# Kernel tuning notes

Hardware: AMD Instinct MI355X
Metric: run time of the kernel (lower is better)

## Reference

```python
import jax, jax.numpy as jnp
import numpy as np

N_SRC0, N_DST0 = 200000, 50000
N_DST1 = 10000
D_IN, D_HID = 128, 128


def _sage_mean(h, src, dst, n_dst, W_self, b_self, W_neigh, b_neigh, act):
    # gather messages from src nodes, mean-aggregate per dst node
    msg = h[src]                                             # [E, D]
    agg = jax.ops.segment_sum(msg, dst, num_segments=n_dst)  # [n_dst, D]
    deg = jax.ops.segment_sum(jnp.ones(dst.shape, h.dtype), dst, num_segments=n_dst)
    h_neigh = agg / jnp.maximum(deg, 1.0)[:, None]
    # DGL block convention: dst nodes are the first n_dst src nodes
    rst = h[:n_dst] @ W_self + b_self + h_neigh @ W_neigh + b_neigh
    return jax.nn.relu(rst) if act else rst


def setup_inputs() -> dict:
    key = jax.random.key(0)
    ks = jax.random.split(key, 12)
    s = 1.0 / np.sqrt(D_HID)
    return {
        "features": jax.random.normal(ks[0], (N_SRC0, D_IN), jnp.float32),
        "src0": jax.random.randint(ks[1], (800000,), 0, N_SRC0),
        "dst0": jax.random.randint(ks[2], (800000,), 0, N_DST0),
        "src1": jax.random.randint(ks[3], (160000,), 0, N_DST0),
        "dst1": jax.random.randint(ks[4], (160000,), 0, N_DST1),
        "W_init": jax.random.uniform(ks[5], (D_IN, D_HID), jnp.float32, -s, s),
        "b_init": jax.random.uniform(ks[6], (D_HID,), jnp.float32, -s, s),
        "W_self": jax.random.uniform(ks[7], (D_HID, D_HID), jnp.float32, -s, s),
        "b_self": jax.random.uniform(ks[8], (D_HID,), jnp.float32, -s, s),
        "W_neigh": jax.random.uniform(ks[9], (D_HID, D_HID), jnp.float32, -s, s),
        "b_neigh": jax.random.uniform(ks[10], (D_HID,), jnp.float32, -s, s),
    }


def reference(features, src0, dst0, src1, dst1, W_init, b_init, W_self, b_self, W_neigh, b_neigh):
    # fc_init + activation
    h = jax.nn.relu(features @ W_init + b_init)              # [N_SRC0, D_HID]
    # block 0 (act_flag True), dropout p=0.0 is identity
    h = _sage_mean(h, src0, dst0, N_DST0, W_self, b_self, W_neigh, b_neigh, act=True)
    # block 1 (last block: act_flag False)
    h = _sage_mean(h, src1, dst1, N_DST1, W_self, b_self, W_neigh, b_neigh, act=False)
    return jnp.squeeze(h, axis=1) if h.shape[1] == 1 else h  # h.squeeze(1) no-op for D_HID>1
```

## Files before the change

kernel.cpp:

```cpp
#include <hip/hip_runtime.h>
#include <stdint.h>
#include <stddef.h>


#define DIM 128
constexpr int N_SRC0 = 200000;
constexpr int N_DST0 = 50000;
constexpr int N_DST1 = 10000;
constexpr int E0 = 800000;
constexpr int E1 = 160000;
constexpr int MAXDEG = 64;

constexpr int FC_BLOCKS = 1024;
constexpr int PLACE_BLOCKS = 1024;

typedef __attribute__((ext_vector_type(8))) short bf16x8;
typedef __attribute__((ext_vector_type(4))) float f32x4;

__device__ __forceinline__ uint16_t f2bf(float f) {
  union { float f; uint32_t u; } v; v.f = f;
  return (uint16_t)((v.u + 0x7FFFu + ((v.u >> 16) & 1u)) >> 16);
}
__device__ __forceinline__ float bf2f(uint16_t h) {
  union { uint32_t u; float f; } v; v.u = ((uint32_t)h) << 16;
  return v.f;
}

__global__ __launch_bounds__(256, 4) void place_fc_kernel(
    const int* __restrict__ src0, const int* __restrict__ dst0,
    const int* __restrict__ src1, const int* __restrict__ dst1,
    int* __restrict__ cnt0, int* __restrict__ cnt1,
    int* __restrict__ eslot0, int* __restrict__ eslot1,
    const float* __restrict__ feat, const float* __restrict__ W_init,
    const float* __restrict__ bias, uint16_t* __restrict__ hout) {
  __shared__ __align__(16) float tile[2][4096];

  if ((blockIdx.x & 1) == 0) {
    int pb = blockIdx.x >> 1;
    int part = pb & 7;
    int bpp  = PLACE_BLOCKS >> 3;
    int bidx = pb >> 3;
    const int4* s04 = (const int4*)src0;
    const int4* d04 = (const int4*)dst0;
    const int4* s14 = (const int4*)src1;
    const int4* d14 = (const int4*)dst1;

    int lo = part * (N_DST0 / 8), hi = lo + (N_DST0 / 8);
    for (int i = bidx * 256 + threadIdx.x; i < E0 / 4; i += bpp * 256) {
      int4 d = d04[i]; int4 s = s04[i];
      if (d.x >= lo && d.x < hi) { int p = atomicAdd(&cnt0[d.x], 1); if (p < MAXDEG) eslot0[(size_t)d.x * MAXDEG + p] = s.x; }
      if (d.y >= lo && d.y < hi) { int p = atomicAdd(&cnt0[d.y], 1); if (p < MAXDEG) eslot0[(size_t)d.y * MAXDEG + p] = s.y; }
      if (d.z >= lo && d.z < hi) { int p = atomicAdd(&cnt0[d.z], 1); if (p < MAXDEG) eslot0[(size_t)d.z * MAXDEG + p] = s.z; }
      if (d.w >= lo && d.w < hi) { int p = atomicAdd(&cnt0[d.w], 1); if (p < MAXDEG) eslot0[(size_t)d.w * MAXDEG + p] = s.w; }
    }
    int lo1 = part * (N_DST1 / 8), hi1 = lo1 + (N_DST1 / 8);
    for (int i = bidx * 256 + threadIdx.x; i < E1 / 4; i += bpp * 256) {
      int4 d = d14[i]; int4 s = s14[i];
      if (d.x >= lo1 && d.x < hi1) { int p = atomicAdd(&cnt1[d.x], 1); if (p < MAXDEG) eslot1[(size_t)d.x * MAXDEG + p] = s.x; }
      if (d.y >= lo1 && d.y < hi1) { int p = atomicAdd(&cnt1[d.y], 1); if (p < MAXDEG) eslot1[(size_t)d.y * MAXDEG + p] = s.y; }
      if (d.z >= lo1 && d.z < hi1) { int p = atomicAdd(&cnt1[d.z], 1); if (p < MAXDEG) eslot1[(size_t)d.z * MAXDEG + p] = s.z; }
      if (d.w >= lo1 && d.w < hi1) { int p = atomicAdd(&cnt1[d.w], 1); if (p < MAXDEG) eslot1[(size_t)d.w * MAXDEG + p] = s.w; }
    }
    return;
  }

  const int tid = threadIdx.x;
  const int w = tid >> 6, lane = tid & 63;
  const int q = lane >> 4, m16 = lane & 15;
  const int sl = w >> 1, nh = w & 1;

  {
    uint16_t* wtmp = (uint16_t*)tile;
    for (int u = 0; u < 8; u++) {
      int c = u * 256 + tid;
      int lane_c = c & 63;
      int nt = (c >> 6) & 7;
      int kc = c >> 9;
      int k0 = kc * 32 + (lane_c >> 4) * 8;
      int n  = nt * 16 + (lane_c & 15);
      bf16x8 frag;
#pragma unroll
      for (int j = 0; j < 8; j++)
        frag[j] = (short)f2bf(W_init[(size_t)(k0 + j) * DIM + n]);
      *(bf16x8*)&wtmp[(size_t)c * 8] = frag;
    }
  }
  __syncthreads();

  bf16x8 wv[4][4];
  {
    const uint16_t* wtmp = (const uint16_t*)tile;
#pragma unroll
    for (int kc = 0; kc < 4; kc++)
#pragma unroll
      for (int jj = 0; jj < 4; jj++)
        wv[kc][jj] = *(const bf16x8*)&wtmp[((kc * 8 + nh * 4 + jj) * 64 + lane) * 8];
  }
  __syncthreads();

  float bv[4];
#pragma unroll
  for (int j = 0; j < 4; j++) bv[j] = bias[(nh * 4 + j) * 16 + m16];

  const int ntiles = N_SRC0 / 32;

  const int lrow0 = w * 8 + (lane >> 5);
  auto stage = [&](int t, int buf) {
#pragma unroll
    for (int i = 0; i < 4; i++) {
      int row = lrow0 + i * 2;
      int g = (lane & 31) ^ (row & 7);
      const float* gs = feat + (size_t)t * 4096 + row * 128 + g * 4;
      float* ld = &tile[buf][w * 1024 + i * 256];
      __builtin_amdgcn_global_load_lds(
          (const __attribute__((address_space(1))) uint32_t*)gs,
          (__attribute__((address_space(3))) uint32_t*)ld,
          16, 0, 0);
    }
  };

  int t = blockIdx.x >> 1;
  int cur = 0;
  if (t < ntiles) stage(t, 0);
  __syncthreads();

  const int trow = sl * 16 + m16;
  const int sw = trow & 7;

  while (t < ntiles) {
    int tn = t + FC_BLOCKS;
    if (tn < ntiles) stage(tn, cur ^ 1);

    f32x4 acc[4];
#pragma unroll
    for (int j = 0; j < 4; j++) acc[j] = (f32x4){0.f, 0.f, 0.f, 0.f};

    const char* rb = (const char*)&tile[cur][0] + trow * 512;
#pragma unroll
    for (int kc = 0; kc < 4; kc++) {
      int g0 = kc * 8 + q * 2;
      float4 x0 = *(const float4*)(rb + ((g0    ) ^ sw) * 16);
      float4 x1 = *(const float4*)(rb + ((g0 + 1) ^ sw) * 16);
      bf16x8 a;
      a[0] = (short)f2bf(x0.x); a[1] = (short)f2bf(x0.y);
      a[2] = (short)f2bf(x0.z); a[3] = (short)f2bf(x0.w);
      a[4] = (short)f2bf(x1.x); a[5] = (short)f2bf(x1.y);
      a[6] = (short)f2bf(x1.z); a[7] = (short)f2bf(x1.w);
#pragma unroll
      for (int j = 0; j < 4; j++)
        acc[j] = __builtin_amdgcn_mfma_f32_16x16x32_bf16(a, wv[kc][j], acc[j], 0, 0, 0);
    }

    int rowb = t * 32 + sl * 16 + q * 4;
#pragma unroll
    for (int j = 0; j < 4; j++)
#pragma unroll
      for (int r = 0; r < 4; r++) {
        float v = fmaxf(acc[j][r] + bv[j], 0.f);
        hout[(size_t)(rowb + r) * DIM + (nh * 4 + j) * 16 + m16] = f2bf(v);
      }

    __syncthreads();
    cur ^= 1;
    t = tn;
  }
}

__global__ __launch_bounds__(256) void agg_kernel(
    const int* __restrict__ eslot, const int* __restrict__ deg,
    const uint16_t* __restrict__ hsrc, uint16_t* __restrict__ hout, int n_dst,
    const float* __restrict__ WS_src, const float* __restrict__ WN_src,
    uint16_t* __restrict__ Wf_out) {
  int nagg = n_dst >> 2;
  if (blockIdx.x >= nagg) {
    int pid = (blockIdx.x - nagg) * 256 + threadIdx.x;
#pragma unroll
    for (int u = 0; u < 4; u++) {
      int gid = pid * 4 + u;
      int m = gid >> 14, idx = gid & 16383;
      const float* W = m ? WN_src : WS_src;
      int j = idx & 7, lane = (idx >> 3) & 63, nt = (idx >> 9) & 7, kc = idx >> 12;
      int k = kc * 32 + (lane >> 4) * 8 + j;
      int n = nt * 16 + (lane & 15);
      Wf_out[gid] = f2bf(W[k * DIM + n]);
    }
    return;
  }

  int d = (blockIdx.x * 256 + threadIdx.x) >> 6;
  int lane = threadIdx.x & 63;
  if (d >= n_dst) return;
  const int* sl = eslot + (size_t)d * MAXDEG;
  int dg = deg[d];
  int dgc = dg < MAXDEG ? dg : MAXDEG;
  int qr = lane >> 4;
  int c  = lane & 15;

  float a0 = 0.f, a1 = 0.f, a2 = 0.f, a3 = 0.f;
  float a4 = 0.f, a5 = 0.f, a6 = 0.f, a7 = 0.f;

#define ACC4(P)                                                          \
  a0 += bf2f((uint16_t)(P).x); a1 += bf2f((uint16_t)((P).x >> 16));      \
  a2 += bf2f((uint16_t)(P).y); a3 += bf2f((uint16_t)((P).y >> 16));      \
  a4 += bf2f((uint16_t)(P).z); a5 += bf2f((uint16_t)((P).z >> 16));      \
  a6 += bf2f((uint16_t)(P).w); a7 += bf2f((uint16_t)((P).w >> 16));

  int e = 0;
  for (; e + 16 <= dgc; e += 16) {
    int s0 = sl[e + qr];
    int s1 = sl[e + 4 + qr];
    int s2 = sl[e + 8 + qr];
    int s3 = sl[e + 12 + qr];
    uint4 p0 = *(const uint4*)(hsrc + (size_t)s0 * DIM + c * 8);
    uint4 p1 = *(const uint4*)(hsrc + (size_t)s1 * DIM + c * 8);
    uint4 p2 = *(const uint4*)(hsrc + (size_t)s2 * DIM + c * 8);
    uint4 p3 = *(const uint4*)(hsrc + (size_t)s3 * DIM + c * 8);
    ACC4(p0); ACC4(p1); ACC4(p2); ACC4(p3);
  }
  for (; e + 8 <= dgc; e += 8) {
    int s0 = sl[e + qr];
    int s1 = sl[e + 4 + qr];
    uint4 p0 = *(const uint4*)(hsrc + (size_t)s0 * DIM + c * 8);
    uint4 p1 = *(const uint4*)(hsrc + (size_t)s1 * DIM + c * 8);
    ACC4(p0); ACC4(p1);
  }
  for (; e + 4 <= dgc; e += 4) {
    int s0 = sl[e + qr];
    uint4 p0 = *(const uint4*)(hsrc + (size_t)s0 * DIM + c * 8);
    ACC4(p0);
  }
  int rem = dgc - e;
  if (qr < rem) {
    int s0 = sl[e + qr];
    uint4 p0 = *(const uint4*)(hsrc + (size_t)s0 * DIM + c * 8);
    ACC4(p0);
  }
#undef ACC4

  a0 += __shfl_xor(a0, 16); a0 += __shfl_xor(a0, 32);
  a1 += __shfl_xor(a1, 16); a1 += __shfl_xor(a1, 32);
  a2 += __shfl_xor(a2, 16); a2 += __shfl_xor(a2, 32);
  a3 += __shfl_xor(a3, 16); a3 += __shfl_xor(a3, 32);
  a4 += __shfl_xor(a4, 16); a4 += __shfl_xor(a4, 32);
  a5 += __shfl_xor(a5, 16); a5 += __shfl_xor(a5, 32);
  a6 += __shfl_xor(a6, 16); a6 += __shfl_xor(a6, 32);
  a7 += __shfl_xor(a7, 16); a7 += __shfl_xor(a7, 32);

  if (qr == 0) {
    float inv = 1.f / fmaxf((float)dg, 1.f);
    uint4 o;
    o.x = (uint32_t)f2bf(a0 * inv) | ((uint32_t)f2bf(a1 * inv) << 16);
    o.y = (uint32_t)f2bf(a2 * inv) | ((uint32_t)f2bf(a3 * inv) << 16);
    o.z = (uint32_t)f2bf(a4 * inv) | ((uint32_t)f2bf(a5 * inv) << 16);
    o.w = (uint32_t)f2bf(a6 * inv) | ((uint32_t)f2bf(a7 * inv) << 16);
    *(uint4*)(hout + (size_t)d * DIM + c * 8) = o;
  }
}

template <bool ACT, bool OUT_BF16>
__global__ __launch_bounds__(256) void sage_kernel(
    const uint16_t* __restrict__ hself, const uint16_t* __restrict__ hneigh,
    const uint16_t* __restrict__ WfS, const uint16_t* __restrict__ WfN,
    const float* __restrict__ bS, const float* __restrict__ bN,
    void* __restrict__ outp, int n_dst) {
  __shared__ uint16_t wS[16384];
  __shared__ uint16_t wN[16384];
  {
    const uint4* gS = (const uint4*)WfS;
    const uint4* gN = (const uint4*)WfN;
    uint4* sS = (uint4*)wS;
    uint4* sN = (uint4*)wN;
    for (int i = threadIdx.x; i < 2048; i += 256) { sS[i] = gS[i]; sN[i] = gN[i]; }
  }
  __syncthreads();

  int wave = (blockIdx.x * 256 + threadIdx.x) >> 6;
  int nwaves = (gridDim.x * 256) >> 6;
  int lane = threadIdx.x & 63;
  int q = lane >> 4, m16 = lane & 15;

  float bv[8];
#pragma unroll
  for (int nt = 0; nt < 8; nt++)
    bv[nt] = bS[nt * 16 + m16] + bN[nt * 16 + m16];

  const int nstrips = n_dst / 16;
  int s = wave;
  bf16x8 XS[4], XN[4];
  if (s < nstrips) {
    size_t ro = (size_t)(s * 16 + m16) * DIM + q * 8;
#pragma unroll
    for (int kc = 0; kc < 4; kc++) {
      XS[kc] = *(const bf16x8*)(hself + ro + kc * 32);
      XN[kc] = *(const bf16x8*)(hneigh + ro + kc * 32);
    }
  }

  while (s < nstrips) {
    int sn = s + nwaves;
    bf16x8 YS[4], YN[4];
    if (sn < nstrips) {
      size_t ro = (size_t)(sn * 16 + m16) * DIM + q * 8;
#pragma unroll
      for (int kc = 0; kc < 4; kc++) {
        YS[kc] = *(const bf16x8*)(hself + ro + kc * 32);
        YN[kc] = *(const bf16x8*)(hneigh + ro + kc * 32);
      }
    }

    f32x4 acc[8];
#pragma unroll
    for (int nt = 0; nt < 8; nt++) acc[nt] = (f32x4){0.f, 0.f, 0.f, 0.f};

#pragma unroll
    for (int kc = 0; kc < 4; kc++) {
#pragma unroll
      for (int nt = 0; nt < 8; nt++) {
        size_t fo = (size_t)((kc * 8 + nt) * 64 + lane) * 8;
        bf16x8 ws = *(const bf16x8*)&wS[fo];
        bf16x8 wn = *(const bf16x8*)&wN[fo];
        acc[nt] = __builtin_amdgcn_mfma_f32_16x16x32_bf16(XS[kc], ws, acc[nt], 0, 0, 0);
        acc[nt] = __builtin_amdgcn_mfma_f32_16x16x32_bf16(XN[kc], wn, acc[nt], 0, 0, 0);
      }
    }

    int m0 = s * 16;
#pragma unroll
    for (int nt = 0; nt < 8; nt++)
#pragma unroll
      for (int r = 0; r < 4; r++) {
        float v = acc[nt][r] + bv[nt];
        if (ACT) v = fmaxf(v, 0.f);
        size_t o = (size_t)(m0 + q * 4 + r) * DIM + nt * 16 + m16;
        if (OUT_BF16) ((uint16_t*)outp)[o] = f2bf(v);
        else          ((float*)outp)[o] = v;
      }

#pragma unroll
    for (int i = 0; i < 4; i++) { XS[i] = YS[i]; XN[i] = YN[i]; }
    s = sn;
  }
}

extern "C" void kernel_launch(void* const* d_in, const int* in_sizes, int n_in,
                              void* d_out, int out_size, void* d_ws, size_t ws_size,
                              hipStream_t stream) {
  const float* feat   = (const float*)d_in[0];
  const int* src0     = (const int*)d_in[1];
  const int* dst0     = (const int*)d_in[2];
  const int* src1     = (const int*)d_in[3];
  const int* dst1     = (const int*)d_in[4];
  const float* W_init = (const float*)d_in[5];
  const float* b_init = (const float*)d_in[6];
  const float* W_self = (const float*)d_in[7];
  const float* b_self = (const float*)d_in[8];
  const float* W_neigh= (const float*)d_in[9];
  const float* b_neigh= (const float*)d_in[10];

  char* ws = (char*)d_ws;
  uint16_t* h     = (uint16_t*)(ws + 0);
  uint16_t* h1    = (uint16_t*)(ws + 51200000);
  uint16_t* hn    = (uint16_t*)(ws + 64000000);
  int*      cnt0  = (int*)(ws + 76800000);
  int*      cnt1  = (int*)(ws + 77000000);
  int*      eslot0= (int*)(ws + 77040000);
  int*      eslot1= (int*)(ws + 89840000);
  uint16_t* WfI   = (uint16_t*)(ws + 92400000);
  uint16_t* WfS   = WfI + 16384;
  uint16_t* WfN   = WfS + 16384;

  hipMemsetAsync(ws + 76800000, 0, 240000, stream);

  place_fc_kernel<<<PLACE_BLOCKS + FC_BLOCKS, 256, 0, stream>>>(
      src0, dst0, src1, dst1, cnt0, cnt1, eslot0, eslot1,
      feat, W_init, b_init, h);

  agg_kernel<<<N_DST0 / 4 + 32, 256, 0, stream>>>(eslot0, cnt0, h, hn, N_DST0,
                                                  W_self, W_neigh, WfS);
  sage_kernel<true, true><<<782, 256, 0, stream>>>(h, hn, WfS, WfN, b_self, b_neigh,
                                                   h1, N_DST0);

  agg_kernel<<<N_DST1 / 4, 256, 0, stream>>>(eslot1, cnt1, h1, hn, N_DST1,
                                             nullptr, nullptr, nullptr);
  sage_kernel<false, false><<<157, 256, 0, stream>>>(h1, hn, WfS, WfN, b_self, b_neigh,
                                                     d_out, N_DST1);
}
```

Measured before the change: 273.2 us.

## Fuse neighbor aggregation with SAGE matmul and move weight prep into FC kernel

Merges the separate aggregation and SAGE linear kernels into one kernel per layer. Each block aggregates 16 destination rows into a swizzled LDS tile and immediately runs the MFMA projection against global pre-swizzled weights, so the intermediate neighbor-mean buffer never makes a round trip through HBM. Weight conversion to bf16 fragment layout moves into extra blocks of the first place/FC kernel. The FC loop also replaces __syncthreads with explicit vmcnt waits plus raw barriers so the prefetch of the next tile can stay in flight. The trade-offs are that weights are now read from global memory per block rather than staged in LDS, and each wave computes only two output column tiles.

```diff
diff --git a/kernel.cpp b/kernel.cpp
--- a/kernel.cpp
+++ b/kernel.cpp
@@ -13,6 +13,7 @@
 
 constexpr int FC_BLOCKS = 1024;
 constexpr int PLACE_BLOCKS = 1024;
+constexpr int PREP_BLOCKS = 16;
 
 typedef __attribute__((ext_vector_type(8))) short bf16x8;
 typedef __attribute__((ext_vector_type(4))) float f32x4;
@@ -32,8 +33,25 @@
     int* __restrict__ cnt0, int* __restrict__ cnt1,
     int* __restrict__ eslot0, int* __restrict__ eslot1,
     const float* __restrict__ feat, const float* __restrict__ W_init,
-    const float* __restrict__ bias, uint16_t* __restrict__ hout) {
+    const float* __restrict__ bias, uint16_t* __restrict__ hout,
+    const float* __restrict__ WS_src, const float* __restrict__ WN_src,
+    uint16_t* __restrict__ Wf_out) {
   __shared__ __align__(16) float tile[2][4096];
+
+  if (blockIdx.x >= PLACE_BLOCKS + FC_BLOCKS) {
+    int pid = (blockIdx.x - (PLACE_BLOCKS + FC_BLOCKS)) * 256 + threadIdx.x;
+#pragma unroll
+    for (int u = 0; u < 8; u++) {
+      int gid = pid * 8 + u;
+      int m = gid >> 14, idx = gid & 16383;
+      const float* W = m ? WN_src : WS_src;
+      int j = idx & 7, lane = (idx >> 3) & 63, nt = (idx >> 9) & 7, kc = idx >> 12;
+      int k = kc * 32 + (lane >> 4) * 8 + j;
+      int n = nt * 16 + (lane & 15);
+      Wf_out[gid] = f2bf(W[k * DIM + n]);
+    }
+    return;
+  }
 
   if ((blockIdx.x & 1) == 0) {
     int pb = blockIdx.x >> 1;
@@ -122,14 +140,20 @@
   int t = blockIdx.x >> 1;
   int cur = 0;
   if (t < ntiles) stage(t, 0);
-  __syncthreads();
 
   const int trow = sl * 16 + m16;
   const int sw = trow & 7;
 
   while (t < ntiles) {
     int tn = t + FC_BLOCKS;
-    if (tn < ntiles) stage(tn, cur ^ 1);
+    if (tn < ntiles) {
+      stage(tn, cur ^ 1);
+      asm volatile("s_waitcnt vmcnt(4)" ::: "memory");
+    } else {
+      asm volatile("s_waitcnt vmcnt(0)" ::: "memory");
+    }
+    __builtin_amdgcn_s_barrier();
+    __builtin_amdgcn_sched_barrier(0);
 
     f32x4 acc[4];
 #pragma unroll
@@ -160,186 +184,141 @@
         hout[(size_t)(rowb + r) * DIM + (nh * 4 + j) * 16 + m16] = f2bf(v);
       }
 
-    __syncthreads();
+    __builtin_amdgcn_s_barrier();
     cur ^= 1;
     t = tn;
   }
 }
 
-__global__ __launch_bounds__(256) void agg_kernel(
+template <bool ACT, bool OUT_BF16>
+__global__ __launch_bounds__(256) void aggsage_kernel(
     const int* __restrict__ eslot, const int* __restrict__ deg,
-    const uint16_t* __restrict__ hsrc, uint16_t* __restrict__ hout, int n_dst,
-    const float* __restrict__ WS_src, const float* __restrict__ WN_src,
-    uint16_t* __restrict__ Wf_out) {
-  int nagg = n_dst >> 2;
-  if (blockIdx.x >= nagg) {
-    int pid = (blockIdx.x - nagg) * 256 + threadIdx.x;
-#pragma unroll
-    for (int u = 0; u < 4; u++) {
-      int gid = pid * 4 + u;
-      int m = gid >> 14, idx = gid & 16383;
-      const float* W = m ? WN_src : WS_src;
-      int j = idx & 7, lane = (idx >> 3) & 63, nt = (idx >> 9) & 7, kc = idx >> 12;
-      int k = kc * 32 + (lane >> 4) * 8 + j;
-      int n = nt * 16 + (lane & 15);
-      Wf_out[gid] = f2bf(W[k * DIM + n]);
-    }
-    return;
-  }
-
-  int d = (blockIdx.x * 256 + threadIdx.x) >> 6;
-  int lane = threadIdx.x & 63;
-  if (d >= n_dst) return;
-  const int* sl = eslot + (size_t)d * MAXDEG;
-  int dg = deg[d];
-  int dgc = dg < MAXDEG ? dg : MAXDEG;
-  int qr = lane >> 4;
-  int c  = lane & 15;
-
-  float a0 = 0.f, a1 = 0.f, a2 = 0.f, a3 = 0.f;
-  float a4 = 0.f, a5 = 0.f, a6 = 0.f, a7 = 0.f;
-
-#define ACC4(P)                                                          \
-  a0 += bf2f((uint16_t)(P).x); a1 += bf2f((uint16_t)((P).x >> 16));      \
-  a2 += bf2f((uint16_t)(P).y); a3 += bf2f((uint16_t)((P).y >> 16));      \
-  a4 += bf2f((uint16_t)(P).z); a5 += bf2f((uint16_t)((P).z >> 16));      \
-  a6 += bf2f((uint16_t)(P).w); a7 += bf2f((uint16_t)((P).w >> 16));
-
-  int e = 0;
-  for (; e + 16 <= dgc; e += 16) {
-    int s0 = sl[e + qr];
-    int s1 = sl[e + 4 + qr];
-    int s2 = sl[e + 8 + qr];
-    int s3 = sl[e + 12 + qr];
-    uint4 p0 = *(const uint4*)(hsrc + (size_t)s0 * DIM + c * 8);
-    uint4 p1 = *(const uint4*)(hsrc + (size_t)s1 * DIM + c * 8);
-    uint4 p2 = *(const uint4*)(hsrc + (size_t)s2 * DIM + c * 8);
-    uint4 p3 = *(const uint4*)(hsrc + (size_t)s3 * DIM + c * 8);
-    ACC4(p0); ACC4(p1); ACC4(p2); ACC4(p3);
-  }
-  for (; e + 8 <= dgc; e += 8) {
-    int s0 = sl[e + qr];
-    int s1 = sl[e + 4 + qr];
-    uint4 p0 = *(const uint4*)(hsrc + (size_t)s0 * DIM + c * 8);
-    uint4 p1 = *(const uint4*)(hsrc + (size_t)s1 * DIM + c * 8);
-    ACC4(p0); ACC4(p1);
-  }
-  for (; e + 4 <= dgc; e += 4) {
-    int s0 = sl[e + qr];
-    uint4 p0 = *(const uint4*)(hsrc + (size_t)s0 * DIM + c * 8);
-    ACC4(p0);
-  }
-  int rem = dgc - e;
-  if (qr < rem) {
-    int s0 = sl[e + qr];
-    uint4 p0 = *(const uint4*)(hsrc + (size_t)s0 * DIM + c * 8);
-    ACC4(p0);
-  }
-#undef ACC4
-
-  a0 += __shfl_xor(a0, 16); a0 += __shfl_xor(a0, 32);
-  a1 += __shfl_xor(a1, 16); a1 += __shfl_xor(a1, 32);
-  a2 += __shfl_xor(a2, 16); a2 += __shfl_xor(a2, 32);
-  a3 += __shfl_xor(a3, 16); a3 += __shfl_xor(a3, 32);
-  a4 += __shfl_xor(a4, 16); a4 += __shfl_xor(a4, 32);
-  a5 += __shfl_xor(a5, 16); a5 += __shfl_xor(a5, 32);
-  a6 += __shfl_xor(a6, 16); a6 += __shfl_xor(a6, 32);
-  a7 += __shfl_xor(a7, 16); a7 += __shfl_xor(a7, 32);
-
-  if (qr == 0) {
-    float inv = 1.f / fmaxf((float)dg, 1.f);
-    uint4 o;
-    o.x = (uint32_t)f2bf(a0 * inv) | ((uint32_t)f2bf(a1 * inv) << 16);
-    o.y = (uint32_t)f2bf(a2 * inv) | ((uint32_t)f2bf(a3 * inv) << 16);
-    o.z = (uint32_t)f2bf(a4 * inv) | ((uint32_t)f2bf(a5 * inv) << 16);
-    o.w = (uint32_t)f2bf(a6 * inv) | ((uint32_t)f2bf(a7 * inv) << 16);
-    *(uint4*)(hout + (size_t)d * DIM + c * 8) = o;
-  }
-}
-
-template <bool ACT, bool OUT_BF16>
-__global__ __launch_bounds__(256) void sage_kernel(
-    const uint16_t* __restrict__ hself, const uint16_t* __restrict__ hneigh,
+    const uint16_t* __restrict__ hgat, const uint16_t* __restrict__ hself,
     const uint16_t* __restrict__ WfS, const uint16_t* __restrict__ WfN,
     const float* __restrict__ bS, const float* __restrict__ bN,
-    void* __restrict__ outp, int n_dst) {
-  __shared__ uint16_t wS[16384];
-  __shared__ uint16_t wN[16384];
+    void* __restrict__ outp) {
+  __shared__ __align__(16) uint16_t hn_tile[16 * 128];
+
+  const int strip = blockIdx.x;
+  const int tid = threadIdx.x;
+  const int w = tid >> 6, lane = tid & 63;
+  const int qr = lane >> 4, c = lane & 15;
+
+  for (int rr = 0; rr < 4; rr++) {
+    int r = w + rr * 4;
+    int d = strip * 16 + r;
+    const int* sl = eslot + (size_t)d * MAXDEG;
+    int dg = deg[d];
+    int dgc = dg < MAXDEG ? dg : MAXDEG;
+
+    float a0 = 0.f, a1 = 0.f, a2 = 0.f, a3 = 0.f;
+    float a4 = 0.f, a5 = 0.f, a6 = 0.f, a7 = 0.f;
+
+#define ACC4(P)                                                          \
+    a0 += bf2f((uint16_t)(P).x); a1 += bf2f((uint16_t)((P).x >> 16));    \
+    a2 += bf2f((uint16_t)(P).y); a3 += bf2f((uint16_t)((P).y >> 16));    \
+    a4 += bf2f((uint16_t)(P).z); a5 += bf2f((uint16_t)((P).z >> 16));    \
+    a6 += bf2f((uint16_t)(P).w); a7 += bf2f((uint16_t)((P).w >> 16));
+
+    int e = 0;
+    for (; e + 16 <= dgc; e += 16) {
+      int s0 = sl[e + qr];
+      int s1 = sl[e + 4 + qr];
+      int s2 = sl[e + 8 + qr];
+      int s3 = sl[e + 12 + qr];
+      uint4 p0 = *(const uint4*)(hgat + (size_t)s0 * DIM + c * 8);
+      uint4 p1 = *(const uint4*)(hgat + (size_t)s1 * DIM + c * 8);
+      uint4 p2 = *(const uint4*)(hgat + (size_t)s2 * DIM + c * 8);
+      uint4 p3 = *(const uint4*)(hgat + (size_t)s3 * DIM + c * 8);
+      ACC4(p0); ACC4(p1); ACC4(p2); ACC4(p3);
+    }
+    for (; e + 8 <= dgc; e += 8) {
+      int s0 = sl[e + qr];
+      int s1 = sl[e + 4 + qr];
+      uint4 p0 = *(const uint4*)(hgat + (size_t)s0 * DIM + c * 8);
+      uint4 p1 = *(const uint4*)(hgat + (size_t)s1 * DIM + c * 8);
+      ACC4(p0); ACC4(p1);
+    }
+    for (; e + 4 <= dgc; e += 4) {
+      int s0 = sl[e + qr];
+      uint4 p0 = *(const uint4*)(hgat + (size_t)s0 * DIM + c * 8);
+      ACC4(p0);
+    }
+    int rem = dgc - e;
+    if (qr < rem) {
+      int s0 = sl[e + qr];
+      uint4 p0 = *(const uint4*)(hgat + (size_t)s0 * DIM + c * 8);
+      ACC4(p0);
+    }
+#undef ACC4
+
+    a0 += __shfl_xor(a0, 16); a0 += __shfl_xor(a0, 32);
+    a1 += __shfl_xor(a1, 16); a1 += __shfl_xor(a1, 32);
+    a2 += __shfl_xor(a2, 16); a2 += __shfl_xor(a2, 32);
+    a3 += __shfl_xor(a3, 16); a3 += __shfl_xor(a3, 32);
+    a4 += __shfl_xor(a4, 16); a4 += __shfl_xor(a4, 32);
+    a5 += __shfl_xor(a5, 16); a5 += __shfl_xor(a5, 32);
+    a6 += __shfl_xor(a6, 16); a6 += __shfl_xor(a6, 32);
+    a7 += __shfl_xor(a7, 16); a7 += __shfl_xor(a7, 32);
+
+    if (qr == 0) {
+      float inv = 1.f / fmaxf((float)dg, 1.f);
+      uint4 o;
+      o.x = (uint32_t)f2bf(a0 * inv) | ((uint32_t)f2bf(a1 * inv) << 16);
+      o.y = (uint32_t)f2bf(a2 * inv) | ((uint32_t)f2bf(a3 * inv) << 16);
+      o.z = (uint32_t)f2bf(a4 * inv) | ((uint32_t)f2bf(a5 * inv) << 16);
+      o.w = (uint32_t)f2bf(a6 * inv) | ((uint32_t)f2bf(a7 * inv) << 16);
+      int g = c ^ (r & 7);
+      *(uint4*)&hn_tile[r * 128 + g * 8] = o;
+    }
+  }
+  __syncthreads();
+
+  const int q = lane >> 4, m16 = lane & 15;
+  const int nt0 = w * 2;
+
+  float bv[2];
+#pragma unroll
+  for (int j = 0; j < 2; j++)
+    bv[j] = bS[(nt0 + j) * 16 + m16] + bN[(nt0 + j) * 16 + m16];
+
+  bf16x8 XS[4], XN[4];
   {
-    const uint4* gS = (const uint4*)WfS;
-    const uint4* gN = (const uint4*)WfN;
-    uint4* sS = (uint4*)wS;
-    uint4* sN = (uint4*)wN;
-    for (int i = threadIdx.x; i < 2048; i += 256) { sS[i] = gS[i]; sN[i] = gN[i]; }
-  }
-  __syncthreads();
-
-  int wave = (blockIdx.x * 256 + threadIdx.x) >> 6;
-  int nwaves = (gridDim.x * 256) >> 6;
-  int lane = threadIdx.x & 63;
-  int q = lane >> 4, m16 = lane & 15;
-
-  float bv[8];
-#pragma unroll
-  for (int nt = 0; nt < 8; nt++)
-    bv[nt] = bS[nt * 16 + m16] + bN[nt * 16 + m16];
-
-  const int nstrips = n_dst / 16;
-  int s = wave;
-  bf16x8 XS[4], XN[4];
-  if (s < nstrips) {
-    size_t ro = (size_t)(s * 16 + m16) * DIM + q * 8;
+    size_t ro = (size_t)(strip * 16 + m16) * DIM + q * 8;
 #pragma unroll
     for (int kc = 0; kc < 4; kc++) {
       XS[kc] = *(const bf16x8*)(hself + ro + kc * 32);
-      XN[kc] = *(const bf16x8*)(hneigh + ro + kc * 32);
-    }
-  }
-
-  while (s < nstrips) {
-    int sn = s + nwaves;
-    bf16x8 YS[4], YN[4];
-    if (sn < nstrips) {
-      size_t ro = (size_t)(sn * 16 + m16) * DIM + q * 8;
-#pragma unroll
-      for (int kc = 0; kc < 4; kc++) {
-        YS[kc] = *(const bf16x8*)(hself + ro + kc * 32);
-        YN[kc] = *(const bf16x8*)(hneigh + ro + kc * 32);
-      }
-    }
-
-    f32x4 acc[8];
-#pragma unroll
-    for (int nt = 0; nt < 8; nt++) acc[nt] = (f32x4){0.f, 0.f, 0.f, 0.f};
-
-#pragma unroll
-    for (int kc = 0; kc < 4; kc++) {
-#pragma unroll
-      for (int nt = 0; nt < 8; nt++) {
-        size_t fo = (size_t)((kc * 8 + nt) * 64 + lane) * 8;
-        bf16x8 ws = *(const bf16x8*)&wS[fo];
-        bf16x8 wn = *(const bf16x8*)&wN[fo];
-        acc[nt] = __builtin_amdgcn_mfma_f32_16x16x32_bf16(XS[kc], ws, acc[nt], 0, 0, 0);
-        acc[nt] = __builtin_amdgcn_mfma_f32_16x16x32_bf16(XN[kc], wn, acc[nt], 0, 0, 0);
-      }
-    }
-
-    int m0 = s * 16;
-#pragma unroll
-    for (int nt = 0; nt < 8; nt++)
-#pragma unroll
-      for (int r = 0; r < 4; r++) {
-        float v = acc[nt][r] + bv[nt];
-        if (ACT) v = fmaxf(v, 0.f);
-        size_t o = (size_t)(m0 + q * 4 + r) * DIM + nt * 16 + m16;
-        if (OUT_BF16) ((uint16_t*)outp)[o] = f2bf(v);
-        else          ((float*)outp)[o] = v;
-      }
-
-#pragma unroll
-    for (int i = 0; i < 4; i++) { XS[i] = YS[i]; XN[i] = YN[i]; }
-    s = sn;
-  }
+      int g = (q + kc * 4) ^ (m16 & 7);
+      XN[kc] = *(const bf16x8*)&hn_tile[m16 * 128 + g * 8];
+    }
+  }
+
+  f32x4 acc[2];
+#pragma unroll
+  for (int j = 0; j < 2; j++) acc[j] = (f32x4){0.f, 0.f, 0.f, 0.f};
+
+#pragma unroll
+  for (int kc = 0; kc < 4; kc++)
+#pragma unroll
+    for (int j = 0; j < 2; j++) {
+      size_t fo = (size_t)((kc * 8 + nt0 + j) * 64 + lane) * 8;
+      bf16x8 ws = *(const bf16x8*)&WfS[fo];
+      bf16x8 wn = *(const bf16x8*)&WfN[fo];
+      acc[j] = __builtin_amdgcn_mfma_f32_16x16x32_bf16(XS[kc], ws, acc[j], 0, 0, 0);
+      acc[j] = __builtin_amdgcn_mfma_f32_16x16x32_bf16(XN[kc], wn, acc[j], 0, 0, 0);
+    }
+
+  int m0 = strip * 16;
+#pragma unroll
+  for (int j = 0; j < 2; j++)
+#pragma unroll
+    for (int r = 0; r < 4; r++) {
+      float v = acc[j][r] + bv[j];
+      if (ACT) v = fmaxf(v, 0.f);
+      size_t o = (size_t)(m0 + q * 4 + r) * DIM + (nt0 + j) * 16 + m16;
+      if (OUT_BF16) ((uint16_t*)outp)[o] = f2bf(v);
+      else          ((float*)outp)[o] = v;
+    }
 }
 
 extern "C" void kernel_launch(void* const* d_in, const int* in_sizes, int n_in,
@@ -360,7 +339,6 @@
   char* ws = (char*)d_ws;
   uint16_t* h     = (uint16_t*)(ws + 0);
   uint16_t* h1    = (uint16_t*)(ws + 51200000);
-  uint16_t* hn    = (uint16_t*)(ws + 64000000);
   int*      cnt0  = (int*)(ws + 76800000);
   int*      cnt1  = (int*)(ws + 77000000);
   int*      eslot0= (int*)(ws + 77040000);
@@ -371,17 +349,13 @@
 
   hipMemsetAsync(ws + 76800000, 0, 240000, stream);
 
-  place_fc_kernel<<<PLACE_BLOCKS + FC_BLOCKS, 256, 0, stream>>>(
+  place_fc_kernel<<<PLACE_BLOCKS + FC_BLOCKS + PREP_BLOCKS, 256, 0, stream>>>(
       src0, dst0, src1, dst1, cnt0, cnt1, eslot0, eslot1,
-      feat, W_init, b_init, h);
-
-  agg_kernel<<<N_DST0 / 4 + 32, 256, 0, stream>>>(eslot0, cnt0, h, hn, N_DST0,
-                                                  W_self, W_neigh, WfS);
-  sage_kernel<true, true><<<782, 256, 0, stream>>>(h, hn, WfS, WfN, b_self, b_neigh,
-                                                   h1, N_DST0);
-
-  agg_kernel<<<N_DST1 / 4, 256, 0, stream>>>(eslot1, cnt1, h1, hn, N_DST1,
-                                             nullptr, nullptr, nullptr);
-  sage_kernel<false, false><<<157, 256, 0, stream>>>(h1, hn, WfS, WfN, b_self, b_neigh,
-                                                     d_out, N_DST1);
-}
+      feat, W_init, b_init, h, W_self, W_neigh, WfS);
+
+  aggsage_kernel<true, true><<<N_DST0 / 16, 256, 0, stream>>>(
+      eslot0, cnt0, h, h, WfS, WfN, b_self, b_neigh, h1);
+
+  aggsage_kernel<false, false><<<N_DST1 / 16, 256, 0, stream>>>(
+      eslot1, cnt1, h1, h1, WfS, WfN, b_self, b_neigh, d_out);
+}
```

After: 277.4 us. About the same (+1.5%).

## Pad degree counters per cache line, move weight prep into first kernel, finer FC waits

Applied to the files above, without the earlier changes.

Degree counters are spread out to 64-byte strides (index shifted by 4) so that atomics on neighbouring destination nodes stop contending on one cache line. This makes the memset larger and moves the workspace offsets. The conversion of the self/neighbour weights to bf16 fragments moves from the aggregation launch into extra blocks of the first fused kernel. The FC loop now waits with explicit vmcnt plus raw barriers, so the next tile's prefetch stays in flight while the current tile is computed.

```diff
diff --git a/kernel.cpp b/kernel.cpp
--- a/kernel.cpp
+++ b/kernel.cpp
@@ -10,9 +10,11 @@
 constexpr int E0 = 800000;
 constexpr int E1 = 160000;
 constexpr int MAXDEG = 64;
+#define CPAD 16
 
 constexpr int FC_BLOCKS = 1024;
 constexpr int PLACE_BLOCKS = 1024;
+constexpr int PREP_BLOCKS = 16;
 
 typedef __attribute__((ext_vector_type(8))) short bf16x8;
 typedef __attribute__((ext_vector_type(4))) float f32x4;
@@ -32,8 +34,25 @@
     int* __restrict__ cnt0, int* __restrict__ cnt1,
     int* __restrict__ eslot0, int* __restrict__ eslot1,
     const float* __restrict__ feat, const float* __restrict__ W_init,
-    const float* __restrict__ bias, uint16_t* __restrict__ hout) {
+    const float* __restrict__ bias, uint16_t* __restrict__ hout,
+    const float* __restrict__ WS_src, const float* __restrict__ WN_src,
+    uint16_t* __restrict__ Wf_out) {
   __shared__ __align__(16) float tile[2][4096];
+
+  if (blockIdx.x >= PLACE_BLOCKS + FC_BLOCKS) {
+    int pid = (blockIdx.x - (PLACE_BLOCKS + FC_BLOCKS)) * 256 + threadIdx.x;
+#pragma unroll
+    for (int u = 0; u < 8; u++) {
+      int gid = pid * 8 + u;
+      int m = gid >> 14, idx = gid & 16383;
+      const float* W = m ? WN_src : WS_src;
+      int j = idx & 7, lane = (idx >> 3) & 63, nt = (idx >> 9) & 7, kc = idx >> 12;
+      int k = kc * 32 + (lane >> 4) * 8 + j;
+      int n = nt * 16 + (lane & 15);
+      Wf_out[gid] = f2bf(W[k * DIM + n]);
+    }
+    return;
+  }
 
   if ((blockIdx.x & 1) == 0) {
     int pb = blockIdx.x >> 1;
@@ -48,18 +67,18 @@
     int lo = part * (N_DST0 / 8), hi = lo + (N_DST0 / 8);
     for (int i = bidx * 256 + threadIdx.x; i < E0 / 4; i += bpp * 256) {
       int4 d = d04[i]; int4 s = s04[i];
-      if (d.x >= lo && d.x < hi) { int p = atomicAdd(&cnt0[d.x], 1); if (p < MAXDEG) eslot0[(size_t)d.x * MAXDEG + p] = s.x; }
-      if (d.y >= lo && d.y < hi) { int p = atomicAdd(&cnt0[d.y], 1); if (p < MAXDEG) eslot0[(size_t)d.y * MAXDEG + p] = s.y; }
-      if (d.z >= lo && d.z < hi) { int p = atomicAdd(&cnt0[d.z], 1); if (p < MAXDEG) eslot0[(size_t)d.z * MAXDEG + p] = s.z; }
-      if (d.w >= lo && d.w < hi) { int p = atomicAdd(&cnt0[d.w], 1); if (p < MAXDEG) eslot0[(size_t)d.w * MAXDEG + p] = s.w; }
+      if (d.x >= lo && d.x < hi) { int p = atomicAdd(&cnt0[d.x << 4], 1); if (p < MAXDEG) eslot0[(size_t)d.x * MAXDEG + p] = s.x; }
+      if (d.y >= lo && d.y < hi) { int p = atomicAdd(&cnt0[d.y << 4], 1); if (p < MAXDEG) eslot0[(size_t)d.y * MAXDEG + p] = s.y; }
+      if (d.z >= lo && d.z < hi) { int p = atomicAdd(&cnt0[d.z << 4], 1); if (p < MAXDEG) eslot0[(size_t)d.z * MAXDEG + p] = s.z; }
+      if (d.w >= lo && d.w < hi) { int p = atomicAdd(&cnt0[d.w << 4], 1); if (p < MAXDEG) eslot0[(size_t)d.w * MAXDEG + p] = s.w; }
     }
     int lo1 = part * (N_DST1 / 8), hi1 = lo1 + (N_DST1 / 8);
     for (int i = bidx * 256 + threadIdx.x; i < E1 / 4; i += bpp * 256) {
       int4 d = d14[i]; int4 s = s14[i];
-      if (d.x >= lo1 && d.x < hi1) { int p = atomicAdd(&cnt1[d.x], 1); if (p < MAXDEG) eslot1[(size_t)d.x * MAXDEG + p] = s.x; }
-      if (d.y >= lo1 && d.y < hi1) { int p = atomicAdd(&cnt1[d.y], 1); if (p < MAXDEG) eslot1[(size_t)d.y * MAXDEG + p] = s.y; }
-      if (d.z >= lo1 && d.z < hi1) { int p = atomicAdd(&cnt1[d.z], 1); if (p < MAXDEG) eslot1[(size_t)d.z * MAXDEG + p] = s.z; }
-      if (d.w >= lo1 && d.w < hi1) { int p = atomicAdd(&cnt1[d.w], 1); if (p < MAXDEG) eslot1[(size_t)d.w * MAXDEG + p] = s.w; }
+      if (d.x >= lo1 && d.x < hi1) { int p = atomicAdd(&cnt1[d.x << 4], 1); if (p < MAXDEG) eslot1[(size_t)d.x * MAXDEG + p] = s.x; }
+      if (d.y >= lo1 && d.y < hi1) { int p = atomicAdd(&cnt1[d.y << 4], 1); if (p < MAXDEG) eslot1[(size_t)d.y * MAXDEG + p] = s.y; }
+      if (d.z >= lo1 && d.z < hi1) { int p = atomicAdd(&cnt1[d.z << 4], 1); if (p < MAXDEG) eslot1[(size_t)d.z * MAXDEG + p] = s.z; }
+      if (d.w >= lo1 && d.w < hi1) { int p = atomicAdd(&cnt1[d.w << 4], 1); if (p < MAXDEG) eslot1[(size_t)d.w * MAXDEG + p] = s.w; }
     }
     return;
   }
@@ -122,14 +141,20 @@
   int t = blockIdx.x >> 1;
   int cur = 0;
   if (t < ntiles) stage(t, 0);
-  __syncthreads();
 
   const int trow = sl * 16 + m16;
   const int sw = trow & 7;
 
   while (t < ntiles) {
     int tn = t + FC_BLOCKS;
-    if (tn < ntiles) stage(tn, cur ^ 1);
+    if (tn < ntiles) {
+      stage(tn, cur ^ 1);
+      asm volatile("s_waitcnt vmcnt(4)" ::: "memory");
+    } else {
+      asm volatile("s_waitcnt vmcnt(0)" ::: "memory");
+    }
+    __builtin_amdgcn_s_barrier();
+    __builtin_amdgcn_sched_barrier(0);
 
     f32x4 acc[4];
 #pragma unroll
@@ -160,7 +185,7 @@
         hout[(size_t)(rowb + r) * DIM + (nh * 4 + j) * 16 + m16] = f2bf(v);
       }
 
-    __syncthreads();
+    __builtin_amdgcn_s_barrier();
     cur ^= 1;
     t = tn;
   }
@@ -168,30 +193,12 @@
 
 __global__ __launch_bounds__(256) void agg_kernel(
     const int* __restrict__ eslot, const int* __restrict__ deg,
-    const uint16_t* __restrict__ hsrc, uint16_t* __restrict__ hout, int n_dst,
-    const float* __restrict__ WS_src, const float* __restrict__ WN_src,
-    uint16_t* __restrict__ Wf_out) {
-  int nagg = n_dst >> 2;
-  if (blockIdx.x >= nagg) {
-    int pid = (blockIdx.x - nagg) * 256 + threadIdx.x;
-#pragma unroll
-    for (int u = 0; u < 4; u++) {
-      int gid = pid * 4 + u;
-      int m = gid >> 14, idx = gid & 16383;
-      const float* W = m ? WN_src : WS_src;
-      int j = idx & 7, lane = (idx >> 3) & 63, nt = (idx >> 9) & 7, kc = idx >> 12;
-      int k = kc * 32 + (lane >> 4) * 8 + j;
-      int n = nt * 16 + (lane & 15);
-      Wf_out[gid] = f2bf(W[k * DIM + n]);
-    }
-    return;
-  }
-
+    const uint16_t* __restrict__ hsrc, uint16_t* __restrict__ hout, int n_dst) {
   int d = (blockIdx.x * 256 + threadIdx.x) >> 6;
   int lane = threadIdx.x & 63;
   if (d >= n_dst) return;
   const int* sl = eslot + (size_t)d * MAXDEG;
-  int dg = deg[d];
+  int dg = deg[d << 4];
   int dgc = dg < MAXDEG ? dg : MAXDEG;
   int qr = lane >> 4;
   int c  = lane & 15;
@@ -362,26 +369,24 @@
   uint16_t* h1    = (uint16_t*)(ws + 51200000);
   uint16_t* hn    = (uint16_t*)(ws + 64000000);
   int*      cnt0  = (int*)(ws + 76800000);
-  int*      cnt1  = (int*)(ws + 77000000);
-  int*      eslot0= (int*)(ws + 77040000);
-  int*      eslot1= (int*)(ws + 89840000);
-  uint16_t* WfI   = (uint16_t*)(ws + 92400000);
+  int*      cnt1  = (int*)(ws + 80000000);
+  int*      eslot0= (int*)(ws + 80640000);
+  int*      eslot1= (int*)(ws + 93440000);
+  uint16_t* WfI   = (uint16_t*)(ws + 96000000);
   uint16_t* WfS   = WfI + 16384;
   uint16_t* WfN   = WfS + 16384;
 
-  hipMemsetAsync(ws + 76800000, 0, 240000, stream);
-
-  place_fc_kernel<<<PLACE_BLOCKS + FC_BLOCKS, 256, 0, stream>>>(
+  hipMemsetAsync(ws + 76800000, 0, 3840000, stream);
+
+  place_fc_kernel<<<PLACE_BLOCKS + FC_BLOCKS + PREP_BLOCKS, 256, 0, stream>>>(
       src0, dst0, src1, dst1, cnt0, cnt1, eslot0, eslot1,
-      feat, W_init, b_init, h);
-
-  agg_kernel<<<N_DST0 / 4 + 32, 256, 0, stream>>>(eslot0, cnt0, h, hn, N_DST0,
-                                                  W_self, W_neigh, WfS);
+      feat, W_init, b_init, h, W_self, W_neigh, WfS);
+
+  agg_kernel<<<N_DST0 / 4, 256, 0, stream>>>(eslot0, cnt0, h, hn, N_DST0);
   sage_kernel<true, true><<<782, 256, 0, stream>>>(h, hn, WfS, WfN, b_self, b_neigh,
                                                    h1, N_DST0);
 
-  agg_kernel<<<N_DST1 / 4, 256, 0, stream>>>(eslot1, cnt1, h1, hn, N_DST1,
-                                             nullptr, nullptr, nullptr);
+  agg_kernel<<<N_DST1 / 4, 256, 0, stream>>>(eslot1, cnt1, h1, hn, N_DST1);
   sage_kernel<false, false><<<157, 256, 0, stream>>>(h1, hn, WfS, WfN, b_self, b_neigh,
                                                      d_out, N_DST1);
 }
```

Result: no change. 278.2 us (+1.8%).
